# Kernel tuning notes

Hardware: AMD Instinct MI355X
Metric: run time of the kernel (lower is better)

## Reference

```python
import jax, jax.numpy as jnp
import numpy as np

N_NODES = 50000
N_EDGES = 800000
IN_F = 128
OUT_F = 64
ALPHA = 0.2  # LeakyReLU negative slope


def setup_inputs() -> dict:
    key = jax.random.key(0)
    k_h, k_e, k_w, k_b, k_a = jax.random.split(key, 5)
    h = jax.random.normal(k_h, (N_NODES, IN_F), dtype=jnp.float32)
    adj = jax.random.randint(k_e, (2, N_EDGES), 0, N_NODES, dtype=jnp.int64)
    # Linear(in_features, out_features): weight [out, in], bias [out]
    W_w = jax.random.normal(k_w, (OUT_F, IN_F), dtype=jnp.float32) * (1.0 / np.sqrt(IN_F))
    W_b = jax.random.normal(k_b, (OUT_F,), dtype=jnp.float32) * 0.01
    a = jax.random.normal(k_a, (1, 2 * OUT_F), dtype=jnp.float32) * (1.0 / np.sqrt(2 * OUT_F))
    return {"h": h, "adj": adj, "W_w": W_w, "W_b": W_b, "a": a}


def reference(h, adj, W_w, W_b, a):
    N = h.shape[0]
    F_out = W_w.shape[0]
    inv_sqrt_f = 1.0 / float(np.sqrt(F_out))

    data = h @ W_w.T + W_b                      # [N, F_out]
    src, dst = adj[0], adj[1]

    # a @ [data[src] || data[dst]]^T  == (data @ a_src)[src] + (data @ a_dst)[dst]
    a_src, a_dst = a[0, :F_out], a[0, F_out:]
    score = (data @ a_src)[src] + (data @ a_dst)[dst]       # [E]
    edge_e = jnp.exp(jax.nn.leaky_relu(score, ALPHA) * inv_sqrt_f)

    # sparse rowsum over source rows (duplicate edges sum, matching COO semantics)
    rowsum = jax.ops.segment_sum(edge_e, src, num_segments=N)  # [N]
    row_zero = rowsum == 0.0
    rowsum = jnp.where(row_zero, 1.0, rowsum)

    # sparse mm: sum_e edge_e * data[dst] into row src; zero rows get a unit self-loop
    h_prime = jax.ops.segment_sum(edge_e[:, None] * data[dst], src, num_segments=N)
    h_prime = h_prime + row_zero[:, None].astype(data.dtype) * data
    return h_prime / rowsum[:, None]
```

## Files before the change

### kernel.cpp

```cpp
#include <hip/hip_runtime.h>
#include <math.h>

#define IN_F 128
#define OUT_F 64
#define ALPHA 0.2f
#define INV_SQRT_F 0.125f
#define CAP 64
#define BINSH 7
#define BINSZ 128
#define CAPB 4096
#define HS 136

typedef _Float16 h8  __attribute__((ext_vector_type(8)));
typedef float    f4  __attribute__((ext_vector_type(4)));

__device__ __forceinline__ float edge_w(float sc) {
    float lr = sc > 0.f ? sc : ALPHA * sc;
    return __expf(lr * INV_SQRT_F);
}

__device__ __forceinline__ h8 cvt8(float4 a, float4 b) {
    h8 r;
    r[0] = (_Float16)a.x; r[1] = (_Float16)a.y;
    r[2] = (_Float16)a.z; r[3] = (_Float16)a.w;
    r[4] = (_Float16)b.x; r[5] = (_Float16)b.y;
    r[6] = (_Float16)b.z; r[7] = (_Float16)b.w;
    return r;
}

__global__ __launch_bounds__(256) void k_p1(
    const float* __restrict__ h, const float* __restrict__ W,
    const float* __restrict__ b, const float* __restrict__ a,
    const int* __restrict__ src, const int* __restrict__ dst,
    int* __restrict__ gcur, unsigned* __restrict__ pk,
    _Float16* __restrict__ data_h,
    float* __restrict__ s_src, float* __restrict__ s_dst,
    int n_nodes, int n_edges, int g_p1)
{
    __shared__ _Float16 wsh[OUT_F * HS];
    __shared__ int hist[512];
    __shared__ int off[512];
    const int tid = threadIdx.x;

    if ((int)blockIdx.x < g_p1) {
        const int nbins = (n_nodes + BINSZ - 1) >> BINSH;
        const int e0 = (int)blockIdx.x * 4096 + tid * 16;

        for (int i = tid; i < nbins; i += 256) hist[i] = 0;
        __syncthreads();

        int s[16], d[16];
        const bool full = (e0 + 16 <= n_edges);
        if (full) {
            #pragma unroll
            for (int c = 0; c < 4; ++c) {
                int4 s4 = *(const int4*)&src[e0 + c * 4];
                int4 d4 = *(const int4*)&dst[e0 + c * 4];
                s[c*4+0] = s4.x; s[c*4+1] = s4.y; s[c*4+2] = s4.z; s[c*4+3] = s4.w;
                d[c*4+0] = d4.x; d[c*4+1] = d4.y; d[c*4+2] = d4.z; d[c*4+3] = d4.w;
            }
            #pragma unroll
            for (int i = 0; i < 16; ++i)
                atomicAdd(&hist[s[i] >> BINSH], 1);
        } else {
            #pragma unroll
            for (int i = 0; i < 16; ++i) {
                int e = e0 + i;
                s[i] = (e < n_edges) ? src[e] : -1;
                d[i] = (e < n_edges) ? dst[e] : 0;
                if (s[i] >= 0) atomicAdd(&hist[s[i] >> BINSH], 1);
            }
        }
        __syncthreads();

        for (int i = tid; i < nbins; i += 256) {
            int c = hist[i];
            off[i] = (c > 0) ? atomicAdd(&gcur[i], c) : 0;
            hist[i] = 0;
        }
        __syncthreads();

        #pragma unroll
        for (int i = 0; i < 16; ++i) {
            if (s[i] < 0) continue;
            int bin = s[i] >> BINSH;
            int r = atomicAdd(&hist[bin], 1);
            int p = off[bin] + r;
            if (p < CAPB)
                pk[(size_t)bin * CAPB + p] =
                    ((unsigned)(s[i] & (BINSZ - 1)) << 16) | (unsigned)d[i];
        }
        return;
    }

    const int node0 = ((int)blockIdx.x - g_p1) * 64;

    for (int i = tid * 8; i < OUT_F * IN_F; i += 2048) {
        int f = i >> 7, k = i & 127;
        float4 va = *(const float4*)&W[i];
        float4 vb = *(const float4*)&W[i + 4];
        *(h8*)&wsh[f * HS + k] = cvt8(va, vb);
    }
    __syncthreads();

    const int wv  = tid >> 6;
    const int lane = tid & 63;
    const int q   = lane >> 4;
    const int col = lane & 15;
    const int r0  = wv * 16;

    const int arow = min(node0 + r0 + col, n_nodes - 1);
    const float* __restrict__ hrow = h + (size_t)arow * IN_F;

    f4 acc[4] = {{0.f,0.f,0.f,0.f},{0.f,0.f,0.f,0.f},
                 {0.f,0.f,0.f,0.f},{0.f,0.f,0.f,0.f}};
    #pragma unroll
    for (int kk = 0; kk < 4; ++kk) {
        const int ko = kk * 32 + q * 8;
        float4 ha = *(const float4*)&hrow[ko];
        float4 hb = *(const float4*)&hrow[ko + 4];
        h8 av = cvt8(ha, hb);
        #pragma unroll
        for (int ct = 0; ct < 4; ++ct) {
            h8 bv = *(const h8*)&wsh[(ct * 16 + col) * HS + ko];
            acc[ct] = __builtin_amdgcn_mfma_f32_16x16x32_f16(av, bv, acc[ct], 0, 0, 0);
        }
    }

    float bb[4], as_[4], ad_[4];
    #pragma unroll
    for (int ct = 0; ct < 4; ++ct) {
        bb[ct]  = b[ct * 16 + col];
        as_[ct] = a[ct * 16 + col];
        ad_[ct] = a[OUT_F + ct * 16 + col];
    }
    #pragma unroll
    for (int reg = 0; reg < 4; ++reg) {
        int n = node0 + r0 + q * 4 + reg;
        float vv[4], ps = 0.f, pd = 0.f;
        #pragma unroll
        for (int ct = 0; ct < 4; ++ct) {
            float v = acc[ct][reg] + bb[ct];
            vv[ct] = v;
            ps = fmaf(v, as_[ct], ps);
            pd = fmaf(v, ad_[ct], pd);
        }
        #pragma unroll
        for (int m = 1; m <= 8; m <<= 1) {
            ps += __shfl_xor(ps, m, 64);
            pd += __shfl_xor(pd, m, 64);
        }
        if (n < n_nodes) {
            size_t base = (size_t)n * OUT_F + col;
            #pragma unroll
            for (int ct = 0; ct < 4; ++ct)
                data_h[base + ct * 16] = (_Float16)vv[ct];
            if (col == 0) { s_src[n] = ps; s_dst[n] = pd; }
        }
    }
}

__global__ __launch_bounds__(512) void k_bin(
    const unsigned* __restrict__ pk, const int* __restrict__ gcur,
    const float* __restrict__ s_src, const float* __restrict__ s_dst,
    const _Float16* __restrict__ data_h, float* __restrict__ out, int n_nodes)
{
    __shared__ unsigned short dbl[64 * CAP];
    __shared__ int lcnt[64];
    const int bin  = (int)blockIdx.x >> 1;
    const int half = (int)blockIdx.x & 1;
    const int tid  = threadIdx.x;

    if (tid < 64) lcnt[tid] = 0;
    __syncthreads();

    const int ecnt = min(gcur[bin], CAPB);
    for (int i = tid; i < ecnt; i += 512) {
        unsigned v = pk[(size_t)bin * CAPB + i];
        int sl = (int)(v >> 16);
        if ((sl >> 6) == half) {
            int r = atomicAdd(&lcnt[sl & 63], 1);
            if (r < CAP) dbl[(sl & 63) * CAP + r] = (unsigned short)(v & 0xffffu);
        }
    }
    __syncthreads();

    const int wv = tid >> 6, lane = tid & 63;
    const int g  = lane >> 3;
    const int fl = lane & 7;

    #pragma unroll 1
    for (int ni = 0; ni < 8; ++ni) {
        const int nl = wv * 8 + ni;
        const int n = bin * BINSZ + half * 64 + nl;
        if (n >= n_nodes) break;
        const int cn = min(lcnt[nl], CAP);
        const float ssrc = s_src[n];
        const int bbase = nl * CAP;

        float ac[8] = {0.f,0.f,0.f,0.f,0.f,0.f,0.f,0.f};
        float rs = 0.f;
        int t = 0;
        for (; t + 16 <= cn; t += 16) {
            int d0 = (int)dbl[bbase + t + g];
            int d1 = (int)dbl[bbase + t + 8 + g];
            float w0 = edge_w(ssrc + s_dst[d0]);
            float w1 = edge_w(ssrc + s_dst[d1]);
            h8 x0 = *(const h8*)&data_h[(size_t)d0 * OUT_F + 8 * fl];
            h8 x1 = *(const h8*)&data_h[(size_t)d1 * OUT_F + 8 * fl];
            #pragma unroll
            for (int i = 0; i < 8; ++i) ac[i] = fmaf(w0, (float)x0[i], ac[i]);
            #pragma unroll
            for (int i = 0; i < 8; ++i) ac[i] = fmaf(w1, (float)x1[i], ac[i]);
            rs += w0 + w1;
        }
        for (; t + 8 <= cn; t += 8) {
            int d0 = (int)dbl[bbase + t + g];
            float w0 = edge_w(ssrc + s_dst[d0]);
            h8 x0 = *(const h8*)&data_h[(size_t)d0 * OUT_F + 8 * fl];
            #pragma unroll
            for (int i = 0; i < 8; ++i) ac[i] = fmaf(w0, (float)x0[i], ac[i]);
            rs += w0;
        }
        const int rem = cn - t;
        if (g < rem) {
            int d0 = (int)dbl[bbase + t + g];
            float w0 = edge_w(ssrc + s_dst[d0]);
            h8 x0 = *(const h8*)&data_h[(size_t)d0 * OUT_F + 8 * fl];
            #pragma unroll
            for (int i = 0; i < 8; ++i) ac[i] = fmaf(w0, (float)x0[i], ac[i]);
            rs += w0;
        }
        #pragma unroll
        for (int m = 8; m <= 32; m <<= 1) {
            #pragma unroll
            for (int i = 0; i < 8; ++i) ac[i] += __shfl_xor(ac[i], m, 64);
            rs += __shfl_xor(rs, m, 64);
        }

        if (g == 0) {
            size_t o = (size_t)n * OUT_F + 8 * fl;
            f4 r0, r1;
            if (rs == 0.f) {
                h8 xv = *(const h8*)&data_h[o];
                r0[0] = (float)xv[0]; r0[1] = (float)xv[1];
                r0[2] = (float)xv[2]; r0[3] = (float)xv[3];
                r1[0] = (float)xv[4]; r1[1] = (float)xv[5];
                r1[2] = (float)xv[6]; r1[3] = (float)xv[7];
            } else {
                float inv = 1.f / rs;
                r0[0] = ac[0] * inv; r0[1] = ac[1] * inv;
                r0[2] = ac[2] * inv; r0[3] = ac[3] * inv;
                r1[0] = ac[4] * inv; r1[1] = ac[5] * inv;
                r1[2] = ac[6] * inv; r1[3] = ac[7] * inv;
            }
            __builtin_nontemporal_store(r0, (f4*)&out[o]);
            __builtin_nontemporal_store(r1, (f4*)&out[o + 4]);
        }
    }
}

extern "C" void kernel_launch(void* const* d_in, const int* in_sizes, int n_in,
                              void* d_out, int out_size, void* d_ws, size_t ws_size,
                              hipStream_t stream)
{
    const float* h   = (const float*)d_in[0];
    const int*   adj = (const int*)  d_in[1];
    const float* W   = (const float*)d_in[2];
    const float* b   = (const float*)d_in[3];
    const float* a   = (const float*)d_in[4];
    float* out = (float*)d_out;

    const int n_nodes = in_sizes[0] / IN_F;
    const int n_edges = in_sizes[1] / 2;
    const int* src = adj;
    const int* dst = adj + n_edges;
    const int nbins = (n_nodes + BINSZ - 1) >> BINSH;

    char* p = (char*)d_ws;
    _Float16*       data_h = (_Float16*)p;       p += (size_t)n_nodes * OUT_F * 2;
    unsigned*       pk     = (unsigned*)p;       p += (size_t)nbins * CAPB * 4;
    float*          s_src  = (float*)p;          p += (size_t)n_nodes * 4;
    float*          s_dst  = (float*)p;          p += (size_t)n_nodes * 4;
    int*            gcur   = (int*)p;            p += (size_t)nbins * 4;

    (void)hipMemsetAsync(gcur, 0, (size_t)nbins * sizeof(int), stream);

    const int g_p1  = (n_edges + 4095) / 4096;
    const int g_lin = (n_nodes + 63) / 64;
    k_p1<<<g_p1 + g_lin, 256, 0, stream>>>(
        h, W, b, a, src, dst, gcur, pk, data_h, s_src, s_dst,
        n_nodes, n_edges, g_p1);

    k_bin<<<nbins * 2, 512, 0, stream>>>(
        pk, gcur, s_src, s_dst, data_h, out, n_nodes);
}
```

Before: 124.6 us.

## Process two node tiles per linear block and precompute edge weights during binning

Each linear-projection block now handles 128 nodes in two passes instead of 64, so the fp16 conversion of W into shared memory is paid once per 128 rows. In the binning kernel, the edge weight is computed while scattering edges into shared lists and stored alongside the destination index as a uint2. The source scores are cached in shared memory. This moves the s_dst gather and exp off the latency-bound aggregation loop, at the cost of doubling shared memory for the edge list (32KB) and possibly lower occupancy.

```diff
diff --git a/kernel.cpp b/kernel.cpp
--- a/kernel.cpp
+++ b/kernel.cpp
@@ -93,7 +93,7 @@
         return;
     }
 
-    const int node0 = ((int)blockIdx.x - g_p1) * 64;
+    const int node0 = ((int)blockIdx.x - g_p1) * 128;
 
     for (int i = tid * 8; i < OUT_F * IN_F; i += 2048) {
         int f = i >> 7, k = i & 127;
@@ -108,24 +108,6 @@
     const int q   = lane >> 4;
     const int col = lane & 15;
     const int r0  = wv * 16;
-
-    const int arow = min(node0 + r0 + col, n_nodes - 1);
-    const float* __restrict__ hrow = h + (size_t)arow * IN_F;
-
-    f4 acc[4] = {{0.f,0.f,0.f,0.f},{0.f,0.f,0.f,0.f},
-                 {0.f,0.f,0.f,0.f},{0.f,0.f,0.f,0.f}};
-    #pragma unroll
-    for (int kk = 0; kk < 4; ++kk) {
-        const int ko = kk * 32 + q * 8;
-        float4 ha = *(const float4*)&hrow[ko];
-        float4 hb = *(const float4*)&hrow[ko + 4];
-        h8 av = cvt8(ha, hb);
-        #pragma unroll
-        for (int ct = 0; ct < 4; ++ct) {
-            h8 bv = *(const h8*)&wsh[(ct * 16 + col) * HS + ko];
-            acc[ct] = __builtin_amdgcn_mfma_f32_16x16x32_f16(av, bv, acc[ct], 0, 0, 0);
-        }
-    }
 
     float bb[4], as_[4], ad_[4];
     #pragma unroll
@@ -134,28 +116,51 @@
         as_[ct] = a[ct * 16 + col];
         ad_[ct] = a[OUT_F + ct * 16 + col];
     }
-    #pragma unroll
-    for (int reg = 0; reg < 4; ++reg) {
-        int n = node0 + r0 + q * 4 + reg;
-        float vv[4], ps = 0.f, pd = 0.f;
+
+    #pragma unroll 1
+    for (int hf = 0; hf < 2; ++hf) {
+        const int nb = node0 + hf * 64;
+        const int arow = min(nb + r0 + col, n_nodes - 1);
+        const float* __restrict__ hrow = h + (size_t)arow * IN_F;
+
+        f4 acc[4] = {{0.f,0.f,0.f,0.f},{0.f,0.f,0.f,0.f},
+                     {0.f,0.f,0.f,0.f},{0.f,0.f,0.f,0.f}};
         #pragma unroll
-        for (int ct = 0; ct < 4; ++ct) {
-            float v = acc[ct][reg] + bb[ct];
-            vv[ct] = v;
-            ps = fmaf(v, as_[ct], ps);
-            pd = fmaf(v, ad_[ct], pd);
-        }
+        for (int kk = 0; kk < 4; ++kk) {
+            const int ko = kk * 32 + q * 8;
+            float4 ha = *(const float4*)&hrow[ko];
+            float4 hb = *(const float4*)&hrow[ko + 4];
+            h8 av = cvt8(ha, hb);
+            #pragma unroll
+            for (int ct = 0; ct < 4; ++ct) {
+                h8 bv = *(const h8*)&wsh[(ct * 16 + col) * HS + ko];
+                acc[ct] = __builtin_amdgcn_mfma_f32_16x16x32_f16(av, bv, acc[ct], 0, 0, 0);
+            }
+        }
+
         #pragma unroll
-        for (int m = 1; m <= 8; m <<= 1) {
-            ps += __shfl_xor(ps, m, 64);
-            pd += __shfl_xor(pd, m, 64);
-        }
-        if (n < n_nodes) {
-            size_t base = (size_t)n * OUT_F + col;
-            #pragma unroll
-            for (int ct = 0; ct < 4; ++ct)
-                data_h[base + ct * 16] = (_Float16)vv[ct];
-            if (col == 0) { s_src[n] = ps; s_dst[n] = pd; }
+        for (int reg = 0; reg < 4; ++reg) {
+            int n = nb + r0 + q * 4 + reg;
+            float vv[4], ps = 0.f, pd = 0.f;
+            #pragma unroll
+            for (int ct = 0; ct < 4; ++ct) {
+                float v = acc[ct][reg] + bb[ct];
+                vv[ct] = v;
+                ps = fmaf(v, as_[ct], ps);
+                pd = fmaf(v, ad_[ct], pd);
+            }
+            #pragma unroll
+            for (int m = 1; m <= 8; m <<= 1) {
+                ps += __shfl_xor(ps, m, 64);
+                pd += __shfl_xor(pd, m, 64);
+            }
+            if (n < n_nodes) {
+                size_t base = (size_t)n * OUT_F + col;
+                #pragma unroll
+                for (int ct = 0; ct < 4; ++ct)
+                    data_h[base + ct * 16] = (_Float16)vv[ct];
+                if (col == 0) { s_src[n] = ps; s_dst[n] = pd; }
+            }
         }
     }
 }
@@ -165,13 +170,19 @@
     const float* __restrict__ s_src, const float* __restrict__ s_dst,
     const _Float16* __restrict__ data_h, float* __restrict__ out, int n_nodes)
 {
-    __shared__ unsigned short dbl[64 * CAP];
-    __shared__ int lcnt[64];
+    __shared__ uint2 edl[64 * CAP];
+    __shared__ int   lcnt[64];
+    __shared__ float ssl[64];
     const int bin  = (int)blockIdx.x >> 1;
     const int half = (int)blockIdx.x & 1;
     const int tid  = threadIdx.x;
-
-    if (tid < 64) lcnt[tid] = 0;
+    const int nbase = bin * BINSZ + half * 64;
+
+    if (tid < 64) {
+        lcnt[tid] = 0;
+        int n = nbase + tid;
+        ssl[tid] = (n < n_nodes) ? s_src[n] : 0.f;
+    }
     __syncthreads();
 
     const int ecnt = min(gcur[bin], CAPB);
@@ -179,8 +190,14 @@
         unsigned v = pk[(size_t)bin * CAPB + i];
         int sl = (int)(v >> 16);
         if ((sl >> 6) == half) {
-            int r = atomicAdd(&lcnt[sl & 63], 1);
-            if (r < CAP) dbl[(sl & 63) * CAP + r] = (unsigned short)(v & 0xffffu);
+            int s63 = sl & 63;
+            int d = (int)(v & 0xffffu);
+            float w = edge_w(ssl[s63] + s_dst[d]);
+            int r = atomicAdd(&lcnt[s63], 1);
+            if (r < CAP) {
+                uint2 e; e.x = (unsigned)d; e.y = __float_as_uint(w);
+                edl[s63 * CAP + r] = e;
+            }
         }
     }
     __syncthreads();
@@ -192,22 +209,21 @@
     #pragma unroll 1
     for (int ni = 0; ni < 8; ++ni) {
         const int nl = wv * 8 + ni;
-        const int n = bin * BINSZ + half * 64 + nl;
+        const int n = nbase + nl;
         if (n >= n_nodes) break;
         const int cn = min(lcnt[nl], CAP);
-        const float ssrc = s_src[n];
         const int bbase = nl * CAP;
 
         float ac[8] = {0.f,0.f,0.f,0.f,0.f,0.f,0.f,0.f};
         float rs = 0.f;
         int t = 0;
         for (; t + 16 <= cn; t += 16) {
-            int d0 = (int)dbl[bbase + t + g];
-            int d1 = (int)dbl[bbase + t + 8 + g];
-            float w0 = edge_w(ssrc + s_dst[d0]);
-            float w1 = edge_w(ssrc + s_dst[d1]);
-            h8 x0 = *(const h8*)&data_h[(size_t)d0 * OUT_F + 8 * fl];
-            h8 x1 = *(const h8*)&data_h[(size_t)d1 * OUT_F + 8 * fl];
+            uint2 e0 = edl[bbase + t + g];
+            uint2 e1 = edl[bbase + t + 8 + g];
+            float w0 = __uint_as_float(e0.y);
+            float w1 = __uint_as_float(e1.y);
+            h8 x0 = *(const h8*)&data_h[(size_t)e0.x * OUT_F + 8 * fl];
+            h8 x1 = *(const h8*)&data_h[(size_t)e1.x * OUT_F + 8 * fl];
             #pragma unroll
             for (int i = 0; i < 8; ++i) ac[i] = fmaf(w0, (float)x0[i], ac[i]);
             #pragma unroll
@@ -215,18 +231,18 @@
             rs += w0 + w1;
         }
         for (; t + 8 <= cn; t += 8) {
-            int d0 = (int)dbl[bbase + t + g];
-            float w0 = edge_w(ssrc + s_dst[d0]);
-            h8 x0 = *(const h8*)&data_h[(size_t)d0 * OUT_F + 8 * fl];
+            uint2 e0 = edl[bbase + t + g];
+            float w0 = __uint_as_float(e0.y);
+            h8 x0 = *(const h8*)&data_h[(size_t)e0.x * OUT_F + 8 * fl];
             #pragma unroll
             for (int i = 0; i < 8; ++i) ac[i] = fmaf(w0, (float)x0[i], ac[i]);
             rs += w0;
         }
         const int rem = cn - t;
         if (g < rem) {
-            int d0 = (int)dbl[bbase + t + g];
-            float w0 = edge_w(ssrc + s_dst[d0]);
-            h8 x0 = *(const h8*)&data_h[(size_t)d0 * OUT_F + 8 * fl];
+            uint2 e0 = edl[bbase + t + g];
+            float w0 = __uint_as_float(e0.y);
+            h8 x0 = *(const h8*)&data_h[(size_t)e0.x * OUT_F + 8 * fl];
             #pragma unroll
             for (int i = 0; i < 8; ++i) ac[i] = fmaf(w0, (float)x0[i], ac[i]);
             rs += w0;
@@ -287,7 +303,7 @@
     (void)hipMemsetAsync(gcur, 0, (size_t)nbins * sizeof(int), stream);
 
     const int g_p1  = (n_edges + 4095) / 4096;
-    const int g_lin = (n_nodes + 63) / 64;
+    const int g_lin = (n_nodes + 127) / 128;
     k_p1<<<g_p1 + g_lin, 256, 0, stream>>>(
         h, W, b, a, src, dst, gcur, pk, data_h, s_src, s_dst,
         n_nodes, n_edges, g_p1);
```

Measured after the change: 130.3 us. +4.6%, slower.
